# Optimization experiments

Hardware: AMD Instinct MI355X
Metric: run time of the kernel (lower is better)

The kernel has to match this reference:

```python
import jax, jax.numpy as jnp
import numpy as np

B, C, T = 1024, 64, 512
D, H = 32, 4
DK = D // H  # 8
EPS = 1e-5


def setup_inputs() -> dict:
    key = jax.random.key(0)
    ks = jax.random.split(key, 10)
    s_in = 1.0 / np.sqrt(T)
    s_d = 1.0 / np.sqrt(D)
    return {
        "x": jax.random.normal(ks[0], (B, C, T), dtype=jnp.float32),
        "W_in": jax.random.uniform(ks[1], (T, D), jnp.float32, -s_in, s_in),
        "b_in": jax.random.uniform(ks[2], (D,), jnp.float32, -s_in, s_in),
        "W_q": jax.random.uniform(ks[3], (D, D), jnp.float32, -s_d, s_d),
        "W_k": jax.random.uniform(ks[4], (D, D), jnp.float32, -s_d, s_d),
        "W_v": jax.random.uniform(ks[5], (D, D), jnp.float32, -s_d, s_d),
        "W_out": jax.random.uniform(ks[6], (D, T), jnp.float32, -s_d, s_d),
        "b_out": jax.random.uniform(ks[7], (T,), jnp.float32, -s_d, s_d),
        "gamma": jnp.ones((T,), jnp.float32),
        "beta": jnp.zeros((T,), jnp.float32),
    }


def reference(x, W_in, b_in, W_q, W_k, W_v, W_out, b_out, gamma, beta):
    # x: (B, C, T) -> project time dim to d_model
    h = jnp.einsum("bct,td->bcd", x, W_in) + b_in  # (B,C,D)
    q = (h @ W_q).reshape(B, C, H, DK)
    k = (h @ W_k).reshape(B, C, H, DK)
    v = (h @ W_v).reshape(B, C, H, DK)
    # attention over channel axis; scores (B,H,C,C)
    scores = jnp.einsum("bchd,bkhd->bhck", q, k) / np.sqrt(DK).astype(np.float32)
    attn = jax.nn.softmax(scores, axis=-1)  # dropout is identity at inference
    out = jnp.einsum("bhck,bkhd->bchd", attn, v).reshape(B, C, D)
    out = out @ W_out + b_out  # (B,C,T); proj_out dropout is identity
    y = out + x  # residual
    mu = jnp.mean(y, axis=-1, keepdims=True)
    var = jnp.var(y, axis=-1, keepdims=True)
    return (y - mu) * jax.lax.rsqrt(var + EPS) * gamma + beta
```

## Files before the change

kernel.cpp:

```cpp
#include <hip/hip_runtime.h>

typedef __attribute__((ext_vector_type(8))) short bf16x8;
typedef __attribute__((ext_vector_type(4))) float f32x4;

#define NB 1024
#define NC 64
#define NT 512
#define ND 32

__device__ __forceinline__ unsigned short f2bf(float f) {
  unsigned u = __float_as_uint(f);
  u += 0x7FFFu + ((u >> 16) & 1u);
  return (unsigned short)(u >> 16);
}

__global__ void prep_weights(const float* __restrict__ Win, const float* __restrict__ Wq,
                             const float* __restrict__ Wk, const float* __restrict__ Wv,
                             const float* __restrict__ Wout, unsigned short* __restrict__ ws) {
  int idx = blockIdx.x * 256 + threadIdx.x;
  if (idx >= 35840) return;
  float v;
  if (idx < 16384) {
    int j = idx & 7, lane = (idx >> 3) & 63, nt = (idx >> 9) & 1, ks = idx >> 10;
    int t = 32 * ks + 8 * (lane >> 4) + j;
    int d = 16 * nt + (lane & 15);
    v = Win[t * ND + d];
  } else if (idx < 32768) {
    int p = idx - 16384;
    int j = p & 7, lane = (p >> 3) & 63, nt = (p >> 9) & 31;
    int k = 8 * (lane >> 4) + j;
    int n = 16 * nt + (lane & 15);
    v = Wout[k * NT + n];
  } else {
    int p = idx - 32768;
    const float* W = (p < 1024) ? Wq : ((p < 2048) ? Wk : Wv);
    int q = p & 1023;
    int j = q & 7, lane = (q >> 3) & 63, nt = (q >> 9) & 1;
    int t = 8 * (lane >> 4) + j;
    int d = 16 * nt + (lane & 15);
    v = W[t * ND + d];
  }
  ws[idx] = f2bf(v);
}

__global__ __launch_bounds__(256, 4)
void mha_main(const float* __restrict__ x, const float* __restrict__ b_in,
              const float* __restrict__ b_out, const float* __restrict__ gamma,
              const float* __restrict__ beta, const unsigned short* __restrict__ wsb,
              float* __restrict__ out) {
  __shared__ __align__(16) unsigned short lds_ho[4][64][8];
  __shared__ __align__(16) float lds_q[64][36];
  __shared__ __align__(16) float lds_k[64][36];
  __shared__ __align__(16) float lds_v[64][36];

  const int tid = threadIdx.x;
  const int w  = tid >> 6;
  const int l  = tid & 63;
  const int g  = l >> 4;
  const int lo = l & 15;
  const int b  = blockIdx.x;
  const float* __restrict__ xb = x + (size_t)b * (NC * NT);

  const int srow = 16 * w + lo;
  const float* __restrict__ xr = xb + srow * NT + 8 * g;
  const bf16x8* __restrict__ wsWin = (const bf16x8*)wsb;

  f32x4 zero4 = (f32x4){0.f, 0.f, 0.f, 0.f};
  f32x4 acc1[2];
  acc1[0] = zero4;
  acc1[1] = zero4;
  f32x4 ra = *(const f32x4*)(xr);
  f32x4 rb = *(const f32x4*)(xr + 4);
  bf16x8 bp0 = wsWin[l];
  bf16x8 bp1 = wsWin[64 + l];

#pragma unroll
  for (int ks = 0; ks < 16; ++ks) {
    bf16x8 af;
    af[0] = (short)f2bf(ra[0]); af[1] = (short)f2bf(ra[1]);
    af[2] = (short)f2bf(ra[2]); af[3] = (short)f2bf(ra[3]);
    af[4] = (short)f2bf(rb[0]); af[5] = (short)f2bf(rb[1]);
    af[6] = (short)f2bf(rb[2]); af[7] = (short)f2bf(rb[3]);
    int nk = (ks < 15) ? (ks + 1) : 15;
    f32x4 ra2 = *(const f32x4*)(xr + 32 * nk);
    f32x4 rb2 = *(const f32x4*)(xr + 32 * nk + 4);
    bf16x8 bn0 = wsWin[(2 * nk) * 64 + l];
    bf16x8 bn1 = wsWin[(2 * nk + 1) * 64 + l];
    acc1[0] = __builtin_amdgcn_mfma_f32_16x16x32_bf16(af, bp0, acc1[0], 0, 0, 0);
    acc1[1] = __builtin_amdgcn_mfma_f32_16x16x32_bf16(af, bp1, acc1[1], 0, 0, 0);
    ra = ra2; rb = rb2; bp0 = bn0; bp1 = bn1;
  }

  float binv0 = b_in[lo];
  float binv1 = b_in[16 + lo];
#pragma unroll
  for (int nt = 0; nt < 2; ++nt) {
#pragma unroll
    for (int r = 0; r < 4; ++r) {
      float hv = acc1[nt][r] + (nt ? binv1 : binv0);
      int cc = 2 * nt + (lo >> 3);
      int slotlane = (4 * g + r) | (cc << 4);
      lds_ho[w][slotlane][lo & 7] = f2bf(hv);
    }
  }
  __syncthreads();

  const bf16x8* __restrict__ wsWq = (const bf16x8*)(wsb + 32768);
  const bf16x8* __restrict__ wsWk = (const bf16x8*)(wsb + 33792);
  const bf16x8* __restrict__ wsWv = (const bf16x8*)(wsb + 34816);
  bf16x8 ah = *(const bf16x8*)&lds_ho[w][l][0];
  f32x4 qacc[2], kacc[2], vacc[2];
#pragma unroll
  for (int nt = 0; nt < 2; ++nt) {
    qacc[nt] = __builtin_amdgcn_mfma_f32_16x16x32_bf16(ah, wsWq[nt * 64 + l], zero4, 0, 0, 0);
    kacc[nt] = __builtin_amdgcn_mfma_f32_16x16x32_bf16(ah, wsWk[nt * 64 + l], zero4, 0, 0, 0);
    vacc[nt] = __builtin_amdgcn_mfma_f32_16x16x32_bf16(ah, wsWv[nt * 64 + l], zero4, 0, 0, 0);
  }
#pragma unroll
  for (int nt = 0; nt < 2; ++nt) {
#pragma unroll
    for (int r = 0; r < 4; ++r) {
      int row = 16 * w + 4 * g + r;
      int col = 16 * nt + lo;
      lds_q[row][col] = qacc[nt][r];
      lds_k[row][col] = kacc[nt][r];
      lds_v[row][col] = vacc[nt][r];
    }
  }
  __syncthreads();

  {
    const int hd = w;
    const f32x4 qv0 = *(const f32x4*)&lds_q[l][8 * hd];
    const f32x4 qv1 = *(const f32x4*)&lds_q[l][8 * hd + 4];
    float sum = 0.f;
    float ov[8] = {0.f, 0.f, 0.f, 0.f, 0.f, 0.f, 0.f, 0.f};
#pragma unroll 4
    for (int kk = 0; kk < 64; ++kk) {
      f32x4 k0 = *(const f32x4*)&lds_k[kk][8 * hd];
      f32x4 k1 = *(const f32x4*)&lds_k[kk][8 * hd + 4];
      float s = qv0[0] * k0[0] + qv0[1] * k0[1] + qv0[2] * k0[2] + qv0[3] * k0[3]
              + qv1[0] * k1[0] + qv1[1] * k1[1] + qv1[2] * k1[2] + qv1[3] * k1[3];
      float p = exp2f(s * (1.4426950408889634f * 0.35355339059327373f));
      sum += p;
      f32x4 v0 = *(const f32x4*)&lds_v[kk][8 * hd];
      f32x4 v1 = *(const f32x4*)&lds_v[kk][8 * hd + 4];
      ov[0] += p * v0[0]; ov[1] += p * v0[1]; ov[2] += p * v0[2]; ov[3] += p * v0[3];
      ov[4] += p * v1[0]; ov[5] += p * v1[1]; ov[6] += p * v1[2]; ov[7] += p * v1[3];
    }
    float inv = 1.0f / sum;
    bf16x8 opk;
#pragma unroll
    for (int d = 0; d < 8; ++d) opk[d] = (short)f2bf(ov[d] * inv);
    *(bf16x8*)&lds_ho[l >> 4][(l & 15) | (hd << 4)][0] = opk;
  }
  __syncthreads();

  const bf16x8 a4 = *(const bf16x8*)&lds_ho[w][l][0];
  const bf16x8* __restrict__ wsWout = (const bf16x8*)(wsb + 16384);
  const int row0 = 16 * w + 4 * g;
  const float* __restrict__ xrow = xb + row0 * NT + lo;

  float s1[4] = {0.f, 0.f, 0.f, 0.f};
  float s2[4] = {0.f, 0.f, 0.f, 0.f};

#pragma unroll 4
  for (int nt = 0; nt < 32; ++nt) {
    bf16x8 bfr = wsWout[nt * 64 + l];
    f32x4 acc = __builtin_amdgcn_mfma_f32_16x16x32_bf16(a4, bfr, zero4, 0, 0, 0);
    int col = 16 * nt;
    float bo = b_out[col + lo];
#pragma unroll
    for (int r = 0; r < 4; ++r) {
      float y = acc[r] + bo + xrow[r * NT + col];
      s1[r] += y;
      s2[r] += y * y;
    }
  }
#pragma unroll
  for (int off = 1; off <= 8; off <<= 1) {
#pragma unroll
    for (int r = 0; r < 4; ++r) {
      s1[r] += __shfl_xor(s1[r], off, 64);
      s2[r] += __shfl_xor(s2[r], off, 64);
    }
  }
  float mu[4], rs[4];
#pragma unroll
  for (int r = 0; r < 4; ++r) {
    mu[r] = s1[r] * (1.0f / 512.0f);
    float var = s2[r] * (1.0f / 512.0f) - mu[r] * mu[r];
    rs[r] = rsqrtf(var + 1e-5f);
  }

  float* __restrict__ orow = out + (size_t)b * (NC * NT) + row0 * NT + lo;
#pragma unroll 4
  for (int nt = 0; nt < 32; ++nt) {
    bf16x8 bfr = wsWout[nt * 64 + l];
    f32x4 acc = __builtin_amdgcn_mfma_f32_16x16x32_bf16(a4, bfr, zero4, 0, 0, 0);
    int col = 16 * nt;
    float bo = b_out[col + lo];
    float gm = gamma[col + lo];
    float bt = beta[col + lo];
#pragma unroll
    for (int r = 0; r < 4; ++r) {
      float y = acc[r] + bo + xrow[r * NT + col];
      orow[r * NT + col] = (y - mu[r]) * rs[r] * gm + bt;
    }
  }
}

extern "C" void kernel_launch(void* const* d_in, const int* in_sizes, int n_in,
                              void* d_out, int out_size, void* d_ws, size_t ws_size,
                              hipStream_t stream) {
  const float* x     = (const float*)d_in[0];
  const float* W_in  = (const float*)d_in[1];
  const float* b_in  = (const float*)d_in[2];
  const float* W_q   = (const float*)d_in[3];
  const float* W_k   = (const float*)d_in[4];
  const float* W_v   = (const float*)d_in[5];
  const float* W_out = (const float*)d_in[6];
  const float* b_out = (const float*)d_in[7];
  const float* gamma = (const float*)d_in[8];
  const float* beta  = (const float*)d_in[9];
  unsigned short* ws = (unsigned short*)d_ws;

  prep_weights<<<140, 256, 0, stream>>>(W_in, W_q, W_k, W_v, W_out, ws);
  mha_main<<<NB, 256, 0, stream>>>(x, b_in, b_out, gamma, beta, ws, (float*)d_out);
}
```

Baseline: 86.53 us.

## Split fused MHA kernel into attention and projection+layernorm kernels

Splits the single fused kernel in two. The first kernel computes the input projection, QKV and attention, then stashes each block's bf16 attention output in the tail of that block's output slice. The second kernel reads the stash back, then runs the output projection, residual add and layernorm without any LDS, which could raise occupancy for the memory-heavy epilogue. The attention thread mapping also changes, so each wave now covers 16 rows across all heads, and one barrier is removed. The cost is an extra kernel launch plus a small global round-trip for the stash.

```diff
diff --git a/kernel.cpp b/kernel.cpp
--- a/kernel.cpp
+++ b/kernel.cpp
@@ -44,11 +44,9 @@
 }
 
 __global__ __launch_bounds__(256, 4)
-void mha_main(const float* __restrict__ x, const float* __restrict__ b_in,
-              const float* __restrict__ b_out, const float* __restrict__ gamma,
-              const float* __restrict__ beta, const unsigned short* __restrict__ wsb,
-              float* __restrict__ out) {
-  __shared__ __align__(16) unsigned short lds_ho[4][64][8];
+void mha_a(const float* __restrict__ x, const float* __restrict__ b_in,
+           const unsigned short* __restrict__ wsb, float* __restrict__ ostash) {
+  __shared__ __align__(16) unsigned short lds_h[4][64][8];
   __shared__ __align__(16) float lds_q[64][36];
   __shared__ __align__(16) float lds_k[64][36];
   __shared__ __align__(16) float lds_v[64][36];
@@ -100,15 +98,14 @@
       float hv = acc1[nt][r] + (nt ? binv1 : binv0);
       int cc = 2 * nt + (lo >> 3);
       int slotlane = (4 * g + r) | (cc << 4);
-      lds_ho[w][slotlane][lo & 7] = f2bf(hv);
-    }
-  }
-  __syncthreads();
+      lds_h[w][slotlane][lo & 7] = f2bf(hv);
+    }
+  }
 
   const bf16x8* __restrict__ wsWq = (const bf16x8*)(wsb + 32768);
   const bf16x8* __restrict__ wsWk = (const bf16x8*)(wsb + 33792);
   const bf16x8* __restrict__ wsWv = (const bf16x8*)(wsb + 34816);
-  bf16x8 ah = *(const bf16x8*)&lds_ho[w][l][0];
+  bf16x8 ah = *(const bf16x8*)&lds_h[w][l][0];
   f32x4 qacc[2], kacc[2], vacc[2];
 #pragma unroll
   for (int nt = 0; nt < 2; ++nt) {
@@ -130,33 +127,52 @@
   __syncthreads();
 
   {
-    const int hd = w;
-    const f32x4 qv0 = *(const f32x4*)&lds_q[l][8 * hd];
-    const f32x4 qv1 = *(const f32x4*)&lds_q[l][8 * hd + 4];
+    const int c = 16 * w + lo;
+    const f32x4 qv0 = *(const f32x4*)&lds_q[c][8 * g];
+    const f32x4 qv1 = *(const f32x4*)&lds_q[c][8 * g + 4];
     float sum = 0.f;
     float ov[8] = {0.f, 0.f, 0.f, 0.f, 0.f, 0.f, 0.f, 0.f};
 #pragma unroll 4
     for (int kk = 0; kk < 64; ++kk) {
-      f32x4 k0 = *(const f32x4*)&lds_k[kk][8 * hd];
-      f32x4 k1 = *(const f32x4*)&lds_k[kk][8 * hd + 4];
+      f32x4 k0 = *(const f32x4*)&lds_k[kk][8 * g];
+      f32x4 k1 = *(const f32x4*)&lds_k[kk][8 * g + 4];
       float s = qv0[0] * k0[0] + qv0[1] * k0[1] + qv0[2] * k0[2] + qv0[3] * k0[3]
               + qv1[0] * k1[0] + qv1[1] * k1[1] + qv1[2] * k1[2] + qv1[3] * k1[3];
       float p = exp2f(s * (1.4426950408889634f * 0.35355339059327373f));
       sum += p;
-      f32x4 v0 = *(const f32x4*)&lds_v[kk][8 * hd];
-      f32x4 v1 = *(const f32x4*)&lds_v[kk][8 * hd + 4];
+      f32x4 v0 = *(const f32x4*)&lds_v[kk][8 * g];
+      f32x4 v1 = *(const f32x4*)&lds_v[kk][8 * g + 4];
       ov[0] += p * v0[0]; ov[1] += p * v0[1]; ov[2] += p * v0[2]; ov[3] += p * v0[3];
       ov[4] += p * v1[0]; ov[5] += p * v1[1]; ov[6] += p * v1[2]; ov[7] += p * v1[3];
     }
     float inv = 1.0f / sum;
-    bf16x8 opk;
-#pragma unroll
-    for (int d = 0; d < 8; ++d) opk[d] = (short)f2bf(ov[d] * inv);
-    *(bf16x8*)&lds_ho[l >> 4][(l & 15) | (hd << 4)][0] = opk;
-  }
+    bf16x8 a4;
+#pragma unroll
+    for (int d = 0; d < 8; ++d) a4[d] = (short)f2bf(ov[d] * inv);
+    bf16x8* __restrict__ stash =
+        (bf16x8*)(ostash + (size_t)b * (NC * NT) + 31744);
+    stash[w * 64 + l] = a4;
+  }
+}
+
+__global__ __launch_bounds__(256, 4)
+void mha_b(const float* __restrict__ x, const float* __restrict__ b_out,
+           const float* __restrict__ gamma, const float* __restrict__ beta,
+           const unsigned short* __restrict__ wsb, float* __restrict__ out) {
+  const int tid = threadIdx.x;
+  const int w  = tid >> 6;
+  const int l  = tid & 63;
+  const int g  = l >> 4;
+  const int lo = l & 15;
+  const int b  = blockIdx.x;
+  const float* __restrict__ xb = x + (size_t)b * (NC * NT);
+  float* __restrict__ ob = out + (size_t)b * (NC * NT);
+
+  const bf16x8* __restrict__ stash = (const bf16x8*)(ob + 31744);
+  const bf16x8 a4 = stash[w * 64 + l];
   __syncthreads();
 
-  const bf16x8 a4 = *(const bf16x8*)&lds_ho[w][l][0];
+  f32x4 zero4 = (f32x4){0.f, 0.f, 0.f, 0.f};
   const bf16x8* __restrict__ wsWout = (const bf16x8*)(wsb + 16384);
   const int row0 = 16 * w + 4 * g;
   const float* __restrict__ xrow = xb + row0 * NT + lo;
@@ -193,7 +209,7 @@
     rs[r] = rsqrtf(var + 1e-5f);
   }
 
-  float* __restrict__ orow = out + (size_t)b * (NC * NT) + row0 * NT + lo;
+  float* __restrict__ orow = ob + row0 * NT + lo;
 #pragma unroll 4
   for (int nt = 0; nt < 32; ++nt) {
     bf16x8 bfr = wsWout[nt * 64 + l];
@@ -226,5 +242,6 @@
   unsigned short* ws = (unsigned short*)d_ws;
 
   prep_weights<<<140, 256, 0, stream>>>(W_in, W_q, W_k, W_v, W_out, ws);
-  mha_main<<<NB, 256, 0, stream>>>(x, b_in, b_out, gamma, beta, ws, (float*)d_out);
-}
+  mha_a<<<NB, 256, 0, stream>>>(x, b_in, ws, (float*)d_out);
+  mha_b<<<NB, 256, 0, stream>>>(x, b_out, gamma, beta, ws, (float*)d_out);
+}
```

Result: slower. 100.8 us (+16.5%).

## Split fused MHA kernel into QKV, attention, and output kernels with finer tiling

Applied to the files above, without the earlier changes.

Replaces the single per-batch kernel with three kernels. k_qkv splits each batch into four channel tiles and splits the K dimension across waves, reducing partial sums through LDS. k_attn runs two blocks per batch, and k_out processes 16-row tiles with a cross-wave LayerNorm reduction. Intermediate Q/K/V and attention outputs are stored as bf16 scratch inside the output buffer. The aim is more blocks and higher occupancy, at the cost of extra launches, intermediate global round-trips and a second full read of x. There is also a possible cross-block race: attention-output stashes overwrite the Q region that the sibling half-block reads.

```diff
diff --git a/kernel.cpp b/kernel.cpp
--- a/kernel.cpp
+++ b/kernel.cpp
@@ -1,6 +1,7 @@
 #include <hip/hip_runtime.h>
 
 typedef __attribute__((ext_vector_type(8))) short bf16x8;
+typedef __attribute__((ext_vector_type(8))) unsigned short u16x8;
 typedef __attribute__((ext_vector_type(4))) float f32x4;
 
 #define NB 1024
@@ -12,6 +13,9 @@
   unsigned u = __float_as_uint(f);
   u += 0x7FFFu + ((u >> 16) & 1u);
   return (unsigned short)(u >> 16);
+}
+__device__ __forceinline__ float bf2f(unsigned short h) {
+  return __uint_as_float(((unsigned)h) << 16);
 }
 
 __global__ void prep_weights(const float* __restrict__ Win, const float* __restrict__ Wq,
@@ -43,133 +47,139 @@
   ws[idx] = f2bf(v);
 }
 
-__global__ __launch_bounds__(256, 4)
-void mha_main(const float* __restrict__ x, const float* __restrict__ b_in,
-              const float* __restrict__ b_out, const float* __restrict__ gamma,
-              const float* __restrict__ beta, const unsigned short* __restrict__ wsb,
-              float* __restrict__ out) {
-  __shared__ __align__(16) unsigned short lds_ho[4][64][8];
-  __shared__ __align__(16) float lds_q[64][36];
-  __shared__ __align__(16) float lds_k[64][36];
-  __shared__ __align__(16) float lds_v[64][36];
-
+__global__ __launch_bounds__(256, 8)
+void k_qkv(const float* __restrict__ x, const float* __restrict__ b_in,
+           const unsigned short* __restrict__ wsb, float* __restrict__ outb) {
+  __shared__ __align__(16) float hp[4][16][32];
+  __shared__ __align__(16) unsigned short hb[16][32];
   const int tid = threadIdx.x;
-  const int w  = tid >> 6;
-  const int l  = tid & 63;
-  const int g  = l >> 4;
-  const int lo = l & 15;
-  const int b  = blockIdx.x;
+  const int w = tid >> 6, l = tid & 63, g = l >> 4, lo = l & 15;
+  const int b = blockIdx.x >> 2, t = blockIdx.x & 3;
   const float* __restrict__ xb = x + (size_t)b * (NC * NT);
 
-  const int srow = 16 * w + lo;
-  const float* __restrict__ xr = xb + srow * NT + 8 * g;
+  const float* __restrict__ xr = xb + (16 * t + lo) * NT + 128 * w + 8 * g;
   const bf16x8* __restrict__ wsWin = (const bf16x8*)wsb;
-
   f32x4 zero4 = (f32x4){0.f, 0.f, 0.f, 0.f};
-  f32x4 acc1[2];
-  acc1[0] = zero4;
-  acc1[1] = zero4;
-  f32x4 ra = *(const f32x4*)(xr);
+  f32x4 acc0 = zero4, acc1 = zero4;
+  f32x4 ra = *(const f32x4*)xr;
   f32x4 rb = *(const f32x4*)(xr + 4);
-  bf16x8 bp0 = wsWin[l];
-  bf16x8 bp1 = wsWin[64 + l];
-
-#pragma unroll
-  for (int ks = 0; ks < 16; ++ks) {
+#pragma unroll
+  for (int i = 0; i < 4; ++i) {
     bf16x8 af;
     af[0] = (short)f2bf(ra[0]); af[1] = (short)f2bf(ra[1]);
     af[2] = (short)f2bf(ra[2]); af[3] = (short)f2bf(ra[3]);
     af[4] = (short)f2bf(rb[0]); af[5] = (short)f2bf(rb[1]);
     af[6] = (short)f2bf(rb[2]); af[7] = (short)f2bf(rb[3]);
-    int nk = (ks < 15) ? (ks + 1) : 15;
-    f32x4 ra2 = *(const f32x4*)(xr + 32 * nk);
-    f32x4 rb2 = *(const f32x4*)(xr + 32 * nk + 4);
-    bf16x8 bn0 = wsWin[(2 * nk) * 64 + l];
-    bf16x8 bn1 = wsWin[(2 * nk + 1) * 64 + l];
-    acc1[0] = __builtin_amdgcn_mfma_f32_16x16x32_bf16(af, bp0, acc1[0], 0, 0, 0);
-    acc1[1] = __builtin_amdgcn_mfma_f32_16x16x32_bf16(af, bp1, acc1[1], 0, 0, 0);
-    ra = ra2; rb = rb2; bp0 = bn0; bp1 = bn1;
-  }
-
-  float binv0 = b_in[lo];
-  float binv1 = b_in[16 + lo];
-#pragma unroll
-  for (int nt = 0; nt < 2; ++nt) {
-#pragma unroll
-    for (int r = 0; r < 4; ++r) {
-      float hv = acc1[nt][r] + (nt ? binv1 : binv0);
-      int cc = 2 * nt + (lo >> 3);
-      int slotlane = (4 * g + r) | (cc << 4);
-      lds_ho[w][slotlane][lo & 7] = f2bf(hv);
-    }
-  }
-  __syncthreads();
-
-  const bf16x8* __restrict__ wsWq = (const bf16x8*)(wsb + 32768);
-  const bf16x8* __restrict__ wsWk = (const bf16x8*)(wsb + 33792);
-  const bf16x8* __restrict__ wsWv = (const bf16x8*)(wsb + 34816);
-  bf16x8 ah = *(const bf16x8*)&lds_ho[w][l][0];
-  f32x4 qacc[2], kacc[2], vacc[2];
-#pragma unroll
-  for (int nt = 0; nt < 2; ++nt) {
-    qacc[nt] = __builtin_amdgcn_mfma_f32_16x16x32_bf16(ah, wsWq[nt * 64 + l], zero4, 0, 0, 0);
-    kacc[nt] = __builtin_amdgcn_mfma_f32_16x16x32_bf16(ah, wsWk[nt * 64 + l], zero4, 0, 0, 0);
-    vacc[nt] = __builtin_amdgcn_mfma_f32_16x16x32_bf16(ah, wsWv[nt * 64 + l], zero4, 0, 0, 0);
-  }
-#pragma unroll
-  for (int nt = 0; nt < 2; ++nt) {
-#pragma unroll
-    for (int r = 0; r < 4; ++r) {
-      int row = 16 * w + 4 * g + r;
-      int col = 16 * nt + lo;
-      lds_q[row][col] = qacc[nt][r];
-      lds_k[row][col] = kacc[nt][r];
-      lds_v[row][col] = vacc[nt][r];
-    }
-  }
-  __syncthreads();
-
+    int ni = (i < 3) ? (i + 1) : 3;
+    f32x4 ra2 = *(const f32x4*)(xr + 32 * ni);
+    f32x4 rb2 = *(const f32x4*)(xr + 32 * ni + 4);
+    int ks = 4 * w + i;
+    acc0 = __builtin_amdgcn_mfma_f32_16x16x32_bf16(af, wsWin[(2 * ks) * 64 + l], acc0, 0, 0, 0);
+    acc1 = __builtin_amdgcn_mfma_f32_16x16x32_bf16(af, wsWin[(2 * ks + 1) * 64 + l], acc1, 0, 0, 0);
+    ra = ra2; rb = rb2;
+  }
+#pragma unroll
+  for (int r = 0; r < 4; ++r) {
+    hp[w][4 * g + r][lo] = acc0[r];
+    hp[w][4 * g + r][16 + lo] = acc1[r];
+  }
+  __syncthreads();
+#pragma unroll
+  for (int e0 = 0; e0 < 2; ++e0) {
+    int e = e0 * 256 + tid;
+    int r = e >> 5, d = e & 31;
+    float s = hp[0][r][d] + hp[1][r][d] + hp[2][r][d] + hp[3][r][d] + b_in[d];
+    hb[r][d] = f2bf(s);
+  }
+  __syncthreads();
+  if (w < 3) {
+    const bf16x8* __restrict__ wsW = (const bf16x8*)(wsb + 32768 + 1024 * w);
+    bf16x8 ah = *(const bf16x8*)&hb[lo][8 * g];
+    unsigned short* __restrict__ u =
+        (unsigned short*)(outb + (size_t)b * (NC * NT)) + 2048 * w;
+#pragma unroll
+    for (int nt = 0; nt < 2; ++nt) {
+      f32x4 qa = __builtin_amdgcn_mfma_f32_16x16x32_bf16(ah, wsW[nt * 64 + l], zero4, 0, 0, 0);
+#pragma unroll
+      for (int r = 0; r < 4; ++r) {
+        int c = 16 * t + 4 * g + r;
+        u[c * 32 + 16 * nt + lo] = f2bf(qa[r]);
+      }
+    }
+  }
+}
+
+__global__ __launch_bounds__(128, 8)
+void k_attn(float* __restrict__ outb) {
+  __shared__ __align__(16) unsigned short qkv[6144];
+  const int tid = threadIdx.x;
+  const int w = tid >> 6, l = tid & 63, g = l >> 4, lo = l & 15;
+  const int b = blockIdx.x >> 1, half = blockIdx.x & 1;
+  unsigned short* __restrict__ u = (unsigned short*)(outb + (size_t)b * (NC * NT));
+#pragma unroll
+  for (int i = 0; i < 6; ++i) {
+    int idx = i * 128 + tid;
+    *(u16x8*)&qkv[8 * idx] = *(const u16x8*)&u[8 * idx];
+  }
+  __syncthreads();
+  const int c = 32 * half + 16 * w + lo;
+  const int hd = g;
+  float qv[8];
   {
-    const int hd = w;
-    const f32x4 qv0 = *(const f32x4*)&lds_q[l][8 * hd];
-    const f32x4 qv1 = *(const f32x4*)&lds_q[l][8 * hd + 4];
-    float sum = 0.f;
-    float ov[8] = {0.f, 0.f, 0.f, 0.f, 0.f, 0.f, 0.f, 0.f};
+    u16x8 q8 = *(const u16x8*)&qkv[c * 32 + 8 * hd];
+#pragma unroll
+    for (int j = 0; j < 8; ++j) qv[j] = bf2f(q8[j]);
+  }
+  float sum = 0.f;
+  float ov[8] = {0.f, 0.f, 0.f, 0.f, 0.f, 0.f, 0.f, 0.f};
 #pragma unroll 4
-    for (int kk = 0; kk < 64; ++kk) {
-      f32x4 k0 = *(const f32x4*)&lds_k[kk][8 * hd];
-      f32x4 k1 = *(const f32x4*)&lds_k[kk][8 * hd + 4];
-      float s = qv0[0] * k0[0] + qv0[1] * k0[1] + qv0[2] * k0[2] + qv0[3] * k0[3]
-              + qv1[0] * k1[0] + qv1[1] * k1[1] + qv1[2] * k1[2] + qv1[3] * k1[3];
-      float p = exp2f(s * (1.4426950408889634f * 0.35355339059327373f));
-      sum += p;
-      f32x4 v0 = *(const f32x4*)&lds_v[kk][8 * hd];
-      f32x4 v1 = *(const f32x4*)&lds_v[kk][8 * hd + 4];
-      ov[0] += p * v0[0]; ov[1] += p * v0[1]; ov[2] += p * v0[2]; ov[3] += p * v0[3];
-      ov[4] += p * v1[0]; ov[5] += p * v1[1]; ov[6] += p * v1[2]; ov[7] += p * v1[3];
-    }
-    float inv = 1.0f / sum;
-    bf16x8 opk;
-#pragma unroll
-    for (int d = 0; d < 8; ++d) opk[d] = (short)f2bf(ov[d] * inv);
-    *(bf16x8*)&lds_ho[l >> 4][(l & 15) | (hd << 4)][0] = opk;
-  }
-  __syncthreads();
-
-  const bf16x8 a4 = *(const bf16x8*)&lds_ho[w][l][0];
+  for (int kk = 0; kk < 64; ++kk) {
+    u16x8 k8 = *(const u16x8*)&qkv[2048 + kk * 32 + 8 * hd];
+    float s = 0.f;
+#pragma unroll
+    for (int j = 0; j < 8; ++j) s += qv[j] * bf2f(k8[j]);
+    float p = exp2f(s * (1.4426950408889634f * 0.35355339059327373f));
+    sum += p;
+    u16x8 v8 = *(const u16x8*)&qkv[4096 + kk * 32 + 8 * hd];
+#pragma unroll
+    for (int j = 0; j < 8; ++j) ov[j] += p * bf2f(v8[j]);
+  }
+  float inv = 1.0f / sum;
+  bf16x8 o8;
+#pragma unroll
+  for (int j = 0; j < 8; ++j) o8[j] = (short)f2bf(ov[j] * inv);
+  const int tt = 2 * half + w;
+  bf16x8* __restrict__ stash = (bf16x8*)(outb + (size_t)b * (NC * NT) + 8192 * tt);
+  stash[16 * g + lo] = o8;
+}
+
+__global__ __launch_bounds__(256, 8)
+void k_out(const float* __restrict__ x, const float* __restrict__ b_out,
+           const float* __restrict__ gamma, const float* __restrict__ beta,
+           const unsigned short* __restrict__ wsb, float* __restrict__ out) {
+  __shared__ float red0[4][16];
+  __shared__ float red1[4][16];
+  __shared__ float mu_a[16], rs_a[16];
+  const int tid = threadIdx.x;
+  const int w = tid >> 6, l = tid & 63, g = l >> 4, lo = l & 15;
+  const int b = blockIdx.x >> 2, t = blockIdx.x & 3;
+  const float* __restrict__ xb = x + (size_t)b * (NC * NT);
+  float* __restrict__ ob = out + (size_t)b * (NC * NT);
+
+  const bf16x8 a4 = ((const bf16x8*)(ob + 8192 * t))[l];
   const bf16x8* __restrict__ wsWout = (const bf16x8*)(wsb + 16384);
-  const int row0 = 16 * w + 4 * g;
-  const float* __restrict__ xrow = xb + row0 * NT + lo;
+  f32x4 zero4 = (f32x4){0.f, 0.f, 0.f, 0.f};
+  const int colbase = 128 * w + lo;
+  const float* __restrict__ xrow = xb + (16 * t + 4 * g) * NT + colbase;
 
   float s1[4] = {0.f, 0.f, 0.f, 0.f};
   float s2[4] = {0.f, 0.f, 0.f, 0.f};
-
 #pragma unroll 4
-  for (int nt = 0; nt < 32; ++nt) {
-    bf16x8 bfr = wsWout[nt * 64 + l];
+  for (int p = 0; p < 8; ++p) {
+    bf16x8 bfr = wsWout[(8 * w + p) * 64 + l];
     f32x4 acc = __builtin_amdgcn_mfma_f32_16x16x32_bf16(a4, bfr, zero4, 0, 0, 0);
-    int col = 16 * nt;
-    float bo = b_out[col + lo];
+    int col = 16 * p;
+    float bo = b_out[colbase + col];
 #pragma unroll
     for (int r = 0; r < 4; ++r) {
       float y = acc[r] + bo + xrow[r * NT + col];
@@ -178,34 +188,39 @@
     }
   }
 #pragma unroll
-  for (int off = 1; off <= 8; off <<= 1) {
+  for (int off = 1; off <= 8; off <<= 1)
 #pragma unroll
     for (int r = 0; r < 4; ++r) {
       s1[r] += __shfl_xor(s1[r], off, 64);
       s2[r] += __shfl_xor(s2[r], off, 64);
     }
-  }
-  float mu[4], rs[4];
-#pragma unroll
-  for (int r = 0; r < 4; ++r) {
-    mu[r] = s1[r] * (1.0f / 512.0f);
-    float var = s2[r] * (1.0f / 512.0f) - mu[r] * mu[r];
-    rs[r] = rsqrtf(var + 1e-5f);
-  }
-
-  float* __restrict__ orow = out + (size_t)b * (NC * NT) + row0 * NT + lo;
+#pragma unroll
+  for (int r = 0; r < 4; ++r)
+    if (lo == r) { red0[w][4 * g + r] = s1[r]; red1[w][4 * g + r] = s2[r]; }
+  __syncthreads();
+  if (tid < 16) {
+    float s = red0[0][tid] + red0[1][tid] + red0[2][tid] + red0[3][tid];
+    float q2 = red1[0][tid] + red1[1][tid] + red1[2][tid] + red1[3][tid];
+    float mu = s * (1.0f / 512.0f);
+    float var = q2 * (1.0f / 512.0f) - mu * mu;
+    mu_a[tid] = mu;
+    rs_a[tid] = rsqrtf(var + 1e-5f);
+  }
+  __syncthreads();
+  float* __restrict__ orow = ob + (16 * t + 4 * g) * NT + colbase;
 #pragma unroll 4
-  for (int nt = 0; nt < 32; ++nt) {
-    bf16x8 bfr = wsWout[nt * 64 + l];
+  for (int p = 0; p < 8; ++p) {
+    bf16x8 bfr = wsWout[(8 * w + p) * 64 + l];
     f32x4 acc = __builtin_amdgcn_mfma_f32_16x16x32_bf16(a4, bfr, zero4, 0, 0, 0);
-    int col = 16 * nt;
-    float bo = b_out[col + lo];
-    float gm = gamma[col + lo];
-    float bt = beta[col + lo];
+    int col = 16 * p;
+    float bo = b_out[colbase + col];
+    float gm = gamma[colbase + col];
+    float bt = beta[colbase + col];
 #pragma unroll
     for (int r = 0; r < 4; ++r) {
       float y = acc[r] + bo + xrow[r * NT + col];
-      orow[r * NT + col] = (y - mu[r]) * rs[r] * gm + bt;
+      int row4 = 4 * g + r;
+      orow[r * NT + col] = (y - mu_a[row4]) * rs_a[row4] * gm + bt;
     }
   }
 }
@@ -226,5 +241,7 @@
   unsigned short* ws = (unsigned short*)d_ws;
 
   prep_weights<<<140, 256, 0, stream>>>(W_in, W_q, W_k, W_v, W_out, ws);
-  mha_main<<<NB, 256, 0, stream>>>(x, b_in, b_out, gamma, beta, ws, (float*)d_out);
-}
+  k_qkv<<<4096, 256, 0, stream>>>(x, b_in, ws, (float*)d_out);
+  k_attn<<<2048, 128, 0, stream>>>((float*)d_out);
+  k_out<<<4096, 256, 0, stream>>>(x, b_out, gamma, beta, ws, (float*)d_out);
+}
```

Result: slower. 143.9 us (+66.3%).
